# Performance work log

Measured on AMD Instinct MI355X. Metric: run time of the kernel, lower is better.

## Reference

```python
import jax, jax.numpy as jnp
import numpy as np
from jax import lax

# 4D convolution via lax.conv_general_dilated (supports N spatial dims natively)
# Layout: x is (N, C, T, U, V, W); weight is (O, I, kT, kU, kV, kW)

def conv4d(x, w, b):
    dn = lax.conv_dimension_numbers(x.shape, w.shape, ('NCTUVW', 'OITUVW', 'NCTUVW'))
    y = lax.conv_general_dilated(x, w, window_strides=(1, 1, 1, 1), padding='SAME',
                                 dimension_numbers=dn)
    return y + b[None, :, None, None, None, None]


def setup_inputs() -> dict:
    key = jax.random.key(0)
    k0, k1, k2, k3, k4 = jax.random.split(key, 5)
    B, C_in, C_hid, C_out = 2, 64, 128, 64
    T, D, H, W = 4, 16, 32, 32
    K = 3  # kernel size per dim (stmode 'C' -> (3,3,3,3))
    x = jax.random.normal(k0, (B, C_in, T, D, H, W), dtype=jnp.float32)
    scale1 = 1.0 / np.sqrt(C_in * K ** 4)
    scale2 = 1.0 / np.sqrt(C_hid * K ** 4)
    w1 = jax.random.normal(k1, (C_hid, C_in, K, K, K, K), dtype=jnp.float32) * scale1
    b1 = jax.random.normal(k2, (C_hid,), dtype=jnp.float32) * scale1
    w2 = jax.random.normal(k3, (C_out, C_hid, K, K, K, K), dtype=jnp.float32) * scale2
    b2 = jax.random.normal(k4, (C_out,), dtype=jnp.float32) * scale2
    return {"x": x, "w1": w1, "b1": b1, "w2": w2, "b2": b2}


def reference(x, w1, b1, w2, b2):
    # conv1 -> ReLU -> (dropout p=0 is identity) -> conv2 -> (dropout identity)
    h = jax.nn.relu(conv4d(x, w1, b1))
    return conv4d(h, w2, b2)
```

## Files before the change

### kernel.cpp

```cpp
#include <hip/hip_runtime.h>


using bf16x8 = __attribute__((ext_vector_type(8))) __bf16;
using f32x16 = __attribute__((ext_vector_type(16))) float;
using f32x4  = __attribute__((ext_vector_type(4))) float;

typedef __attribute__((address_space(1))) const void as1_void;
typedef __attribute__((address_space(3))) void as3_void;
__device__ __forceinline__ void gload_lds16(const void* g, void* l) {
    __builtin_amdgcn_global_load_lds((as1_void*)g, (as3_void*)l, 16, 0, 0);
}

__global__ __launch_bounds__(256) void cvt_x(const float* __restrict__ x,
                                             __bf16* __restrict__ x_t) {
    __shared__ float lt[64][65];
    const int nb = blockIdx.y;
    const int p0 = blockIdx.x * 64;
    const float* src = x + (size_t)nb * 64 * 65536;
    __bf16* dst = x_t + (size_t)nb * 65536 * 64;
    #pragma unroll
    for (int i = 0; i < 16; ++i) {
        int idx = i * 256 + threadIdx.x;
        int c = idx >> 6, p = idx & 63;
        lt[c][p] = src[(size_t)c * 65536 + p0 + p];
    }
    __syncthreads();
    #pragma unroll
    for (int i = 0; i < 16; ++i) {
        int idx = i * 256 + threadIdx.x;
        int p = idx >> 6, c = idx & 63;
        dst[(size_t)(p0 + p) * 64 + c] = (__bf16)lt[c][p];
    }
}

template <int CIN>
__global__ __launch_bounds__(256) void cvt_w(const float* __restrict__ w,
                                             __bf16* __restrict__ wt) {
    constexpr int LOG = (CIN == 64) ? 6 : 7;
    constexpr int COUT = 8192 / CIN;
    int oc = blockIdx.x * 256 + threadIdx.x;
    if (oc >= 8192) return;
    const int o = oc >> LOG, c = oc & (CIN - 1);
    const int kg = c >> 4, cl = c & 15;
    const float* src = w + (size_t)oc * 81;
    #pragma unroll 1
    for (int tap = 0; tap < 81; ++tap)
        wt[(((size_t)tap * (CIN / 16) + kg) * COUT + o) * 16 + cl] = (__bf16)src[tap];
}

template <int CIN, int COUT, int NT, int CHALVES, bool RELU>
__global__ __launch_bounds__(256, 2) void conv4d_mfma(
    const __bf16* __restrict__ in_t,
    const __bf16* __restrict__ wt,
    const float* __restrict__ bias,
    __bf16* __restrict__ out_bf,
    float* __restrict__ out_f,
    const __bf16* __restrict__ zp)
{
    constexpr int KST = CIN / 16;
    __shared__ __bf16 tile[3072 * 8];

    const int tid  = threadIdx.x;
    const int lane = tid & 63;
    const int l31  = lane & 31;
    const int hl   = lane >> 5;
    const int wv   = tid >> 6;
    const int gmi  = wv >> 1;
    const int gni  = wv & 1;

    const int bid = blockIdx.x;
    const int xcd = bid & 7;
    const int s   = bid >> 3;
    const int u   = xcd * 2 + (s & 1);
    const int vg  = (s >> 1) & 3;
    const int t   = (s >> 3) & 3;
    const int nb  = (s >> 5) & 1;
    const int v0  = vg * 8;
    const int pbase = ((t * 16 + u) * 32 + v0) * 32;

    const __bf16* inb = in_t + (size_t)nb * 65536 * CIN;

    int goff[12];
    #pragma unroll
    for (int it = 0; it < 12; ++it) {
        const int idx = it * 256 + tid;
        const int row = idx / 272;
        const int rem = idx - row * 272;
        const int chunk = rem / 34;
        const int wp  = rem - chunk * 34;
        const int v_in = v0 - 1 + row;
        const int w_in = wp - 1;
        const bool ok = (row < 10) && ((unsigned)v_in < 32u) && ((unsigned)w_in < 32u);
        goff[it] = ok ? ((v_in * 32 + w_in) * CIN + chunk * 8) : -1;
    }

    const bf16x8* tile16 = (const bf16x8*)tile;
    const bf16x8* abase[3];
    #pragma unroll
    for (int kw = 0; kw < 3; ++kw)
        abase[kw] = tile16 + (gmi * 1088 + hl * 34 + l31 + kw);

    const __bf16* wlane[NT];
    #pragma unroll
    for (int nt = 0; nt < NT; ++nt)
        wlane[nt] = wt + ((gni * NT + nt) * 32 + l31) * 16 + hl * 8;

    f32x16 acc[4][NT];
    #pragma unroll
    for (int mt = 0; mt < 4; ++mt)
        #pragma unroll
        for (int nt = 0; nt < NT; ++nt)
            #pragma unroll
            for (int i = 0; i < 16; ++i)
                acc[mt][nt][i] = 0.f;

    #pragma unroll 1
    for (int kt = 0; kt < 3; ++kt) {
        const int t_in = t + kt - 1;
        if ((unsigned)t_in >= 4u) continue;
        #pragma unroll 1
        for (int ku = 0; ku < 3; ++ku) {
            const int u_in = u + ku - 1;
            if ((unsigned)u_in >= 16u) continue;
            const int tapbase = (kt * 3 + ku) * 9;
            const __bf16* gstage0 = inb + (size_t)((t_in * 16 + u_in) * 1024) * CIN;
            #pragma unroll 1
            for (int ch = 0; ch < CHALVES; ++ch) {
                const __bf16* gstage = gstage0 + ch * 64;
                __syncthreads();
                #pragma unroll
                for (int it = 0; it < 12; ++it) {
                    const __bf16* gp = (goff[it] >= 0) ? (gstage + goff[it]) : zp;
                    char* lp = ((char*)tile) + it * 4096 + wv * 1024;
                    gload_lds16(gp, lp);
                }
                __syncthreads();
                #pragma unroll
                for (int ks = 0; ks < 4; ++ks) {
                    const int ksg = ch * 4 + ks;
                    bf16x8 af[6][3];
                    #pragma unroll
                    for (int r = 0; r < 6; ++r)
                        #pragma unroll
                        for (int kw = 0; kw < 3; ++kw)
                            af[r][kw] = abase[kw][r * 272 + ks * 68];
                    #pragma unroll
                    for (int kv = 0; kv < 3; ++kv)
                        #pragma unroll
                        for (int kw = 0; kw < 3; ++kw) {
                            const size_t wo =
                                ((size_t)(tapbase + kv * 3 + kw) * KST + ksg) *
                                (COUT * 16);
                            bf16x8 bv[NT];
                            #pragma unroll
                            for (int nt = 0; nt < NT; ++nt)
                                bv[nt] = *(const bf16x8*)(wlane[nt] + wo);
                            #pragma unroll
                            for (int r = kv; r < kv + 4; ++r)
                                #pragma unroll
                                for (int nt = 0; nt < NT; ++nt)
                                    acc[r - kv][nt] =
                                        __builtin_amdgcn_mfma_f32_32x32x16_bf16(
                                            af[r][kw], bv[nt], acc[r - kv][nt],
                                            0, 0, 0);
                        }
                }
            }
        }
    }

    #pragma unroll
    for (int nt = 0; nt < NT; ++nt) {
        const int o = (gni * NT + nt) * 32 + l31;
        const float bv = bias[o];
        #pragma unroll
        for (int mt = 0; mt < 4; ++mt) {
            const int pb = pbase + (gmi * 4 + mt) * 32;
            if constexpr (RELU) {
                #pragma unroll
                for (int rg = 0; rg < 4; ++rg)
                    #pragma unroll
                    for (int j = 0; j < 4; ++j) {
                        float v = acc[mt][nt][rg * 4 + j] + bv;
                        v = v > 0.f ? v : 0.f;
                        const int p = pb + j + 8 * rg + 4 * hl;
                        out_bf[(size_t)(nb * 65536 + p) * COUT + o] = (__bf16)v;
                    }
            } else {
                #pragma unroll
                for (int rg = 0; rg < 4; ++rg) {
                    f32x4 sv;
                    #pragma unroll
                    for (int j = 0; j < 4; ++j)
                        sv[j] = acc[mt][nt][rg * 4 + j] + bv;
                    const int p = pb + 8 * rg + 4 * hl;
                    *(f32x4*)(out_f + ((size_t)nb * COUT + o) * 65536 + p) = sv;
                }
            }
        }
    }
}

extern "C" void kernel_launch(void* const* d_in, const int* in_sizes, int n_in,
                              void* d_out, int out_size, void* d_ws, size_t ws_size,
                              hipStream_t stream) {
    const float* x  = (const float*)d_in[0];
    const float* w1 = (const float*)d_in[1];
    const float* b1 = (const float*)d_in[2];
    const float* w2 = (const float*)d_in[3];
    const float* b2 = (const float*)d_in[4];
    float* out = (float*)d_out;

    char* ws = (char*)d_ws;
    __bf16* x_t = (__bf16*)ws;
    __bf16* h_t = (__bf16*)(ws + 16777216);
    __bf16* w1t = (__bf16*)(ws + 50331648);
    __bf16* w2t = (__bf16*)(ws + 51658752);
    __bf16* zp  = (__bf16*)(ws + 52985856);

    hipMemsetAsync(zp, 0, 256, stream);
    cvt_x<<<dim3(1024, 2), 256, 0, stream>>>(x, x_t);
    cvt_w<64><<<32, 256, 0, stream>>>(w1, w1t);
    cvt_w<128><<<32, 256, 0, stream>>>(w2, w2t);

    conv4d_mfma<64, 128, 2, 1, true><<<512, 256, 0, stream>>>(x_t, w1t, b1, h_t,
                                                              nullptr, zp);
    conv4d_mfma<128, 64, 1, 2, false><<<512, 256, 0, stream>>>(h_t, w2t, b2, nullptr,
                                                               out, zp);
}
```

Baseline: 402.8 us.

## Double-buffer LDS input tiles in 32-channel units with prefetch of next stage

Flattens the (kt,ku,channel-chunk) loops into one linear loop over 32-channel units and double-buffers the LDS tile, issuing the async global-to-LDS loads for the next unit before computing the current one. This removes one barrier per iteration and is meant to overlap global load latency with MFMA work. The inner loop is also reordered to load A fragments per kw and B fragments for all three kv up front. Per-stage work shrinks, so barriers become more frequent, and the larger register footprint (up to 9 offsets plus more B fragments) may pressure occupancy under launch_bounds(256,2).

```diff
diff --git a/kernel.cpp b/kernel.cpp
--- a/kernel.cpp
+++ b/kernel.cpp
@@ -48,7 +48,7 @@
         wt[(((size_t)tap * (CIN / 16) + kg) * COUT + o) * 16 + cl] = (__bf16)src[tap];
 }
 
-template <int CIN, int COUT, int NT, int CHALVES, bool RELU>
+template <int CIN, int COUT, int NT, bool RELU>
 __global__ __launch_bounds__(256, 2) void conv4d_mfma(
     const __bf16* __restrict__ in_t,
     const __bf16* __restrict__ wt,
@@ -57,8 +57,10 @@
     float* __restrict__ out_f,
     const __bf16* __restrict__ zp)
 {
-    constexpr int KST = CIN / 16;
-    __shared__ __bf16 tile[3072 * 8];
+    constexpr int KST   = CIN / 16;
+    constexpr int UNITS = CIN / 32;
+    constexpr int LOGU  = (UNITS == 2) ? 1 : 2;
+    __shared__ __bf16 tile[2 * 12288];
 
     const int tid  = threadIdx.x;
     const int lane = tid & 63;
@@ -70,40 +72,53 @@
 
     const int bid = blockIdx.x;
     const int xcd = bid & 7;
-    const int s   = bid >> 3;
-    const int u   = xcd * 2 + (s & 1);
-    const int vg  = (s >> 1) & 3;
-    const int t   = (s >> 3) & 3;
-    const int nb  = (s >> 5) & 1;
+    const int s0  = bid >> 3;
+    const int u   = xcd * 2 + (s0 & 1);
+    const int vg  = (s0 >> 1) & 3;
+    const int t   = (s0 >> 3) & 3;
+    const int nb  = (s0 >> 5) & 1;
     const int v0  = vg * 8;
     const int pbase = ((t * 16 + u) * 32 + v0) * 32;
 
     const __bf16* inb = in_t + (size_t)nb * 65536 * CIN;
 
-    int goff[12];
-    #pragma unroll
-    for (int it = 0; it < 12; ++it) {
-        const int idx = it * 256 + tid;
-        const int row = idx / 272;
-        const int rem = idx - row * 272;
+    int goff[6];
+    #pragma unroll
+    for (int r = 0; r < 6; ++r) {
+        const int slot = r * 256 + tid;
+        const int row  = slot / 136;
+        const int rem  = slot - row * 136;
         const int chunk = rem / 34;
-        const int wp  = rem - chunk * 34;
+        const int wp   = rem - chunk * 34;
         const int v_in = v0 - 1 + row;
         const int w_in = wp - 1;
         const bool ok = (row < 10) && ((unsigned)v_in < 32u) && ((unsigned)w_in < 32u);
-        goff[it] = ok ? ((v_in * 32 + w_in) * CIN + chunk * 8) : -1;
-    }
-
+        goff[r] = ok ? ((v_in * 32 + w_in) * CIN + chunk * 8) : -1;
+    }
+
+    const int lane_base = (gmi * 16 + hl) * 34 + l31;
     const bf16x8* tile16 = (const bf16x8*)tile;
-    const bf16x8* abase[3];
-    #pragma unroll
-    for (int kw = 0; kw < 3; ++kw)
-        abase[kw] = tile16 + (gmi * 1088 + hl * 34 + l31 + kw);
 
     const __bf16* wlane[NT];
     #pragma unroll
     for (int nt = 0; nt < NT; ++nt)
         wlane[nt] = wt + ((gni * NT + nt) * 32 + l31) * 16 + hl * 8;
+
+    int sb[9], tb0[9], nst = 0;
+    #pragma unroll
+    for (int kt = 0; kt < 3; ++kt) {
+        const int t_in = t + kt - 1;
+        if ((unsigned)t_in >= 4u) continue;
+        #pragma unroll
+        for (int ku = 0; ku < 3; ++ku) {
+            const int u_in = u + ku - 1;
+            if ((unsigned)u_in >= 16u) continue;
+            sb[nst]  = (t_in * 16 + u_in) * 1024 * CIN;
+            tb0[nst] = (kt * 3 + ku) * 9;
+            ++nst;
+        }
+    }
+    const int U = nst * UNITS;
 
     f32x16 acc[4][NT];
     #pragma unroll
@@ -114,57 +129,52 @@
             for (int i = 0; i < 16; ++i)
                 acc[mt][nt][i] = 0.f;
 
+    auto issue = [&](int j) {
+        const int st = j >> LOGU, ch = j & (UNITS - 1);
+        const __bf16* gb = inb + sb[st] + ch * 32;
+        char* lb = ((char*)tile) + (j & 1) * 24576 + wv * 1024;
+        #pragma unroll
+        for (int r = 0; r < 6; ++r) {
+            const __bf16* gp = (goff[r] >= 0) ? (gb + goff[r]) : zp;
+            gload_lds16(gp, lb + r * 4096);
+        }
+    };
+
+    issue(0);
     #pragma unroll 1
-    for (int kt = 0; kt < 3; ++kt) {
-        const int t_in = t + kt - 1;
-        if ((unsigned)t_in >= 4u) continue;
-        #pragma unroll 1
-        for (int ku = 0; ku < 3; ++ku) {
-            const int u_in = u + ku - 1;
-            if ((unsigned)u_in >= 16u) continue;
-            const int tapbase = (kt * 3 + ku) * 9;
-            const __bf16* gstage0 = inb + (size_t)((t_in * 16 + u_in) * 1024) * CIN;
-            #pragma unroll 1
-            for (int ch = 0; ch < CHALVES; ++ch) {
-                const __bf16* gstage = gstage0 + ch * 64;
-                __syncthreads();
-                #pragma unroll
-                for (int it = 0; it < 12; ++it) {
-                    const __bf16* gp = (goff[it] >= 0) ? (gstage + goff[it]) : zp;
-                    char* lp = ((char*)tile) + it * 4096 + wv * 1024;
-                    gload_lds16(gp, lp);
+    for (int i = 0; i < U; ++i) {
+        __syncthreads();
+        if (i + 1 < U) issue(i + 1);
+
+        const int st = i >> LOGU, ch = i & (UNITS - 1);
+        const int tapb = tb0[st];
+        const bf16x8* tb = tile16 + (i & 1) * 1536 + lane_base;
+        #pragma unroll
+        for (int ks = 0; ks < 2; ++ks) {
+            const int ksg = ch * 2 + ks;
+            #pragma unroll
+            for (int kw = 0; kw < 3; ++kw) {
+                bf16x8 af[6];
+                #pragma unroll
+                for (int r = 0; r < 6; ++r)
+                    af[r] = tb[kw + 34 * (4 * r + 2 * ks)];
+                bf16x8 bv[3][NT];
+                #pragma unroll
+                for (int kv = 0; kv < 3; ++kv) {
+                    const size_t wo =
+                        ((size_t)(tapb + kv * 3 + kw) * KST + ksg) * (COUT * 16);
+                    #pragma unroll
+                    for (int nt = 0; nt < NT; ++nt)
+                        bv[kv][nt] = *(const bf16x8*)(wlane[nt] + wo);
                 }
-                __syncthreads();
-                #pragma unroll
-                for (int ks = 0; ks < 4; ++ks) {
-                    const int ksg = ch * 4 + ks;
-                    bf16x8 af[6][3];
-                    #pragma unroll
-                    for (int r = 0; r < 6; ++r)
+                #pragma unroll
+                for (int kv = 0; kv < 3; ++kv)
+                    #pragma unroll
+                    for (int rr = 0; rr < 4; ++rr)
                         #pragma unroll
-                        for (int kw = 0; kw < 3; ++kw)
-                            af[r][kw] = abase[kw][r * 272 + ks * 68];
-                    #pragma unroll
-                    for (int kv = 0; kv < 3; ++kv)
-                        #pragma unroll
-                        for (int kw = 0; kw < 3; ++kw) {
-                            const size_t wo =
-                                ((size_t)(tapbase + kv * 3 + kw) * KST + ksg) *
-                                (COUT * 16);
-                            bf16x8 bv[NT];
-                            #pragma unroll
-                            for (int nt = 0; nt < NT; ++nt)
-                                bv[nt] = *(const bf16x8*)(wlane[nt] + wo);
-                            #pragma unroll
-                            for (int r = kv; r < kv + 4; ++r)
-                                #pragma unroll
-                                for (int nt = 0; nt < NT; ++nt)
-                                    acc[r - kv][nt] =
-                                        __builtin_amdgcn_mfma_f32_32x32x16_bf16(
-                                            af[r][kw], bv[nt], acc[r - kv][nt],
-                                            0, 0, 0);
-                        }
-                }
+                        for (int nt = 0; nt < NT; ++nt)
+                            acc[rr][nt] = __builtin_amdgcn_mfma_f32_32x32x16_bf16(
+                                af[kv + rr], bv[kv][nt], acc[rr][nt], 0, 0, 0);
             }
         }
     }
@@ -172,7 +182,7 @@
     #pragma unroll
     for (int nt = 0; nt < NT; ++nt) {
         const int o = (gni * NT + nt) * 32 + l31;
-        const float bv = bias[o];
+        const float bvls = bias[o];
         #pragma unroll
         for (int mt = 0; mt < 4; ++mt) {
             const int pb = pbase + (gmi * 4 + mt) * 32;
@@ -181,7 +191,7 @@
                 for (int rg = 0; rg < 4; ++rg)
                     #pragma unroll
                     for (int j = 0; j < 4; ++j) {
-                        float v = acc[mt][nt][rg * 4 + j] + bv;
+                        float v = acc[mt][nt][rg * 4 + j] + bvls;
                         v = v > 0.f ? v : 0.f;
                         const int p = pb + j + 8 * rg + 4 * hl;
                         out_bf[(size_t)(nb * 65536 + p) * COUT + o] = (__bf16)v;
@@ -192,7 +202,7 @@
                     f32x4 sv;
                     #pragma unroll
                     for (int j = 0; j < 4; ++j)
-                        sv[j] = acc[mt][nt][rg * 4 + j] + bv;
+                        sv[j] = acc[mt][nt][rg * 4 + j] + bvls;
                     const int p = pb + 8 * rg + 4 * hl;
                     *(f32x4*)(out_f + ((size_t)nb * COUT + o) * 65536 + p) = sv;
                 }
@@ -223,8 +233,8 @@
     cvt_w<64><<<32, 256, 0, stream>>>(w1, w1t);
     cvt_w<128><<<32, 256, 0, stream>>>(w2, w2t);
 
-    conv4d_mfma<64, 128, 2, 1, true><<<512, 256, 0, stream>>>(x_t, w1t, b1, h_t,
-                                                              nullptr, zp);
-    conv4d_mfma<128, 64, 1, 2, false><<<512, 256, 0, stream>>>(h_t, w2t, b2, nullptr,
-                                                               out, zp);
-}
+    conv4d_mfma<64, 128, 2, true><<<512, 256, 0, stream>>>(x_t, w1t, b1, h_t,
+                                                           nullptr, zp);
+    conv4d_mfma<128, 64, 1, false><<<512, 256, 0, stream>>>(h_t, w2t, b2, nullptr,
+                                                            out, zp);
+}
```

Result: slower. 415.6 us (+3.2%).
